# Performance work log

Hardware: AMD Instinct MI355X
Metric: run time of the kernel (lower is better)

Reference implementation:

```python
import jax, jax.numpy as jnp
import numpy as np

Q = 128


def _maxpool2(x):
    # 2x2 max pool, stride 2, NCHW
    return jax.lax.reduce_window(x, -jnp.inf, jax.lax.max,
                                 (1, 1, 2, 2), (1, 1, 2, 2), 'VALID')


def _conv(x, w, b):
    y = jax.lax.conv_general_dilated(x, w, window_strides=(1, 1), padding='VALID',
                                     dimension_numbers=('NCHW', 'OIHW', 'NCHW'))
    return y + b[None, :, None, None]


def setup_inputs() -> dict:
    key = jax.random.key(0)
    ks = jax.random.split(key, 16)
    B = 4096
    x = jax.random.normal(ks[0], (B, 1, 28, 28), dtype=jnp.float32)
    hash_idx1 = jax.random.randint(ks[1], (25,), 0, Q, dtype=jnp.int32)
    hash_idx2 = jax.random.randint(ks[2], (800,), 0, Q, dtype=jnp.int32)
    hash_idx3 = jax.random.randint(ks[3], (1024,), 0, Q, dtype=jnp.int32)
    # random +/-1 signs
    sgn1 = jnp.sign(jax.random.normal(ks[4], (25,), dtype=jnp.float32))
    sgn2 = jnp.sign(jax.random.normal(ks[5], (800,), dtype=jnp.float32))
    sgn3 = jnp.sign(jax.random.normal(ks[6], (1024,), dtype=jnp.float32))
    # compressed (sketched) parameters: one length-Q vector per output unit
    w1 = jax.random.normal(ks[7], (32, Q), dtype=jnp.float32) * 0.2
    b1 = jax.random.normal(ks[8], (32,), dtype=jnp.float32) * 0.05
    w2 = jax.random.normal(ks[9], (64, Q), dtype=jnp.float32) * 0.05
    b2 = jax.random.normal(ks[10], (64,), dtype=jnp.float32) * 0.05
    w3 = jax.random.normal(ks[11], (512, Q), dtype=jnp.float32) * 0.03
    b3 = jax.random.normal(ks[12], (512,), dtype=jnp.float32) * 0.05
    fc2_w = jax.random.normal(ks[13], (10, 512), dtype=jnp.float32) * 0.04
    fc2_b = jax.random.normal(ks[14], (10,), dtype=jnp.float32) * 0.05
    return {'x': x,
            'hash_idx1': hash_idx1, 'hash_idx2': hash_idx2, 'hash_idx3': hash_idx3,
            'sgn1': sgn1, 'sgn2': sgn2, 'sgn3': sgn3,
            'w1': w1, 'b1': b1, 'w2': w2, 'b2': b2, 'w3': w3, 'b3': b3,
            'fc2_w': fc2_w, 'fc2_b': fc2_b}


def reference(x, hash_idx1, hash_idx2, hash_idx3, sgn1, sgn2, sgn3,
              w1, b1, w2, b2, w3, b3, fc2_w, fc2_b):
    # SketchConv1: reconstruct dense weight via gather + sign flip
    wc1 = (w1[:, hash_idx1] * sgn1[None, :]).reshape(32, 1, 5, 5)
    h = jax.nn.relu(_maxpool2(_conv(x, wc1, b1)))          # (B,32,12,12)
    # SketchConv2
    wc2 = (w2[:, hash_idx2] * sgn2[None, :]).reshape(64, 32, 5, 5)
    h = jax.nn.relu(_maxpool2(_conv(h, wc2, b2)))          # (B,64,4,4)
    h = h.reshape(h.shape[0], -1)                          # (B,1024)
    # SketchLinear
    W3 = w3[:, hash_idx3] * sgn3[None, :]                  # (512,1024)
    h = jax.nn.relu(h @ W3.T + b3)                         # (B,512)
    logits = h @ fc2_w.T + fc2_b                           # (B,10)
    return jax.nn.log_softmax(logits, axis=1)
```

## Files before the change

kernel.cpp:

```cpp
#include <hip/hip_runtime.h>
#include <hip/hip_bf16.h>
#include <math.h>


typedef __attribute__((ext_vector_type(8))) short bf16x8;
typedef __attribute__((ext_vector_type(4))) float f32x4;

static __device__ inline ushort f2bfu(float v) {
    union { __hip_bfloat16 h; ushort u; } cv;
    cv.h = __float2bfloat16(v);
    return cv.u;
}


__global__ __launch_bounds__(256)
void k_reconstruct(const float* __restrict__ w1, const float* __restrict__ w2,
                   const float* __restrict__ w3,
                   const int* __restrict__ hi1, const int* __restrict__ hi2,
                   const int* __restrict__ hi3,
                   const float* __restrict__ s1, const float* __restrict__ s2,
                   const float* __restrict__ s3,
                   __hip_bfloat16* __restrict__ wc1f,
                   __hip_bfloat16* __restrict__ wc1s,
                   __hip_bfloat16* __restrict__ wc2f,
                   __hip_bfloat16* __restrict__ W3f) {
    const int t = blockIdx.x * blockDim.x + threadIdx.x;
    const int f = t >> 2;
    const int j0 = (t & 3) * 2;
    if (f < 256) {
        const bool shifted = f >= 128;
        const int u = f & 127;
        const int nt = u >> 6, lane = u & 63;
        const int quad = lane >> 4, l15 = lane & 15;
        const int oc = nt * 16 + l15;
        ushort rr[2];
        #pragma unroll
        for (int jj = 0; jj < 2; ++jj) {
            int tt = quad * 8 + j0 + jj;
            int ki = (tt * 43) >> 8;
            int kj = tt - 6 * ki;
            float v = 0.f;
            if (!shifted && ki < 5 && kj < 5) {
                int fi = ki * 5 + kj;
                v = w1[oc * 128 + hi1[fi]] * s1[fi];
            } else if (shifted && ki < 5 && kj >= 1 && kj <= 5) {
                int fi = ki * 5 + (kj - 1);
                v = w1[oc * 128 + hi1[fi]] * s1[fi];
            }
            rr[jj] = f2bfu(v);
        }
        *(uint*)((ushort*)(shifted ? wc1s : wc1f) + (size_t)u * 8 + j0) =
            (uint)rr[0] | ((uint)rr[1] << 16);
    } else if (f < 6656) {
        const int u = f - 256;
        const int l15 = u & 15, quad = (u >> 4) & 3;
        const int ntA = (u >> 6) & 3, tap = u >> 8;
        const int oc = ntA * 16 + l15;
        ushort rr[2];
        #pragma unroll
        for (int jj = 0; jj < 2; ++jj) {
            int ic = quad * 8 + j0 + jj;
            int fi = ic * 25 + tap;
            rr[jj] = f2bfu(w2[oc * 128 + hi2[fi]] * s2[fi]);
        }
        *(uint*)((ushort*)wc2f + (size_t)u * 8 + j0) =
            (uint)rr[0] | ((uint)rr[1] << 16);
    } else if (f < 72192) {
        const int u = f - 6656;
        const int l15 = u & 15, quad = (u >> 4) & 3;
        const int kt = (u >> 6) & 31, ntile = u >> 11;
        const int n = ntile * 16 + l15;
        ushort rr[2];
        #pragma unroll
        for (int jj = 0; jj < 2; ++jj) {
            int k = kt * 32 + quad * 8 + j0 + jj;
            rr[jj] = f2bfu(w3[n * 128 + hi3[k]] * s3[k]);
        }
        *(uint*)((ushort*)W3f + (size_t)u * 8 + j0) =
            (uint)rr[0] | ((uint)rr[1] << 16);
    }
}

__global__ __launch_bounds__(512, 6)
void k_conv(const float* __restrict__ x,
            const __hip_bfloat16* __restrict__ wc1f,
            const __hip_bfloat16* __restrict__ wc1s,
            const __hip_bfloat16* __restrict__ wc2f,
            const float* __restrict__ b1, const float* __restrict__ b2,
            __hip_bfloat16* __restrict__ h2) {
    __shared__ __align__(16) ushort s_xb[4 * 816];
    __shared__ __align__(16) ushort s_h1[16 * 1160];

    const int tid = threadIdx.x;
    const int b0 = blockIdx.x * 4;
    const int wave = tid >> 6, lane = tid & 63;
    const int l15 = lane & 15, quad = lane >> 4;

    {
        const float4* xg = (const float4*)(x + (size_t)b0 * 784);
        for (int i = tid; i < 784; i += 512) {
            float4 v = xg[i];
            int img = i / 196;
            int pos = (i - img * 196) * 4;
            ushort* dst = &s_xb[img * 816 + pos];
            dst[0] = f2bfu(v.x); dst[1] = f2bfu(v.y);
            dst[2] = f2bfu(v.z); dst[3] = f2bfu(v.w);
        }
        if (tid < 128) {
            int img = tid >> 5, k = tid & 31;
            s_xb[img * 816 + 784 + k] = 0;
        }
    }

    bf16x8 bw1[2], bw1s[2];
    float bb1[2];
    #pragma unroll
    for (int nt = 0; nt < 2; ++nt) {
        bw1[nt]  = *(const bf16x8*)((const ushort*)wc1f + (nt * 64 + lane) * 8);
        bw1s[nt] = *(const bf16x8*)((const ushort*)wc1s + (nt * 64 + lane) * 8);
        bb1[nt] = b1[nt * 16 + l15];
    }
    __syncthreads();

    {
        const int img = wave >> 1, half = wave & 1;
        const int sub = l15 & 3;
        const ushort* srcImg = s_xb + img * 816;
        int offr[4];
        #pragma unroll
        for (int r = 0; r < 4; ++r) {
            int t = quad * 8 + 2 * r;
            int row = (t * 43) >> 8;
            int col = t - 6 * row;
            offr[r] = row * 28 + col;
        }
        const int g0 = l15 >> 3, r0 = l15 & 7;
        #pragma unroll
        for (int ii = 0; ii < 18; ++ii) {
            const int i = half * 18 + ii;
            const int pb = 4 * i + (l15 >> 2);
            const int pi = (pb * 171) >> 11;
            const int pj = pb - 12 * pi;
            const int base_e = (2 * pi + (sub >> 1)) * 28 + 2 * pj;
            const ushort* p0 = srcImg + base_e;
            union { bf16x8 v; uint u[4]; } A;
            A.u[0] = *(const uint*)(p0 + offr[0]);
            A.u[1] = *(const uint*)(p0 + offr[1]);
            A.u[2] = *(const uint*)(p0 + offr[2]);
            A.u[3] = *(const uint*)(p0 + offr[3]);
            f32x4 z = {0.f, 0.f, 0.f, 0.f};
            f32x4 ce0 = __builtin_amdgcn_mfma_f32_16x16x32_bf16(A.v, bw1[0],  z, 0, 0, 0);
            f32x4 co0 = __builtin_amdgcn_mfma_f32_16x16x32_bf16(A.v, bw1s[0], z, 0, 0, 0);
            f32x4 ce1 = __builtin_amdgcn_mfma_f32_16x16x32_bf16(A.v, bw1[1],  z, 0, 0, 0);
            f32x4 co1 = __builtin_amdgcn_mfma_f32_16x16x32_bf16(A.v, bw1s[1], z, 0, 0, 0);
            const int pbo = 4 * i + quad;
            float m0 = fmaxf(fmaxf(ce0[0], co0[1]), fmaxf(ce0[2], co0[3]));
            float m1 = fmaxf(fmaxf(ce1[0], co1[1]), fmaxf(ce1[2], co1[3]));
            s_h1[(img * 4 + g0) * 1160 + pbo * 8 + r0]     = f2bfu(fmaxf(m0 + bb1[0], 0.f));
            s_h1[(img * 4 + 2 + g0) * 1160 + pbo * 8 + r0] = f2bfu(fmaxf(m1 + bb1[1], 0.f));
        }
    }
    __syncthreads();

    const int pr = wave >> 1, nh = wave & 1;
    const int sub2 = l15 & 3;
    const int ci2 = 2 * pr + (sub2 >> 1);
    const int cj2 = 2 * (l15 >> 2) + (sub2 & 1);
    const int posBase = (ci2 * 12 + cj2) * 8;

    f32x4 acc[4][2];
    float bb2[2];
    #pragma unroll
    for (int ntl = 0; ntl < 2; ++ntl) {
        bb2[ntl] = b2[(nh * 2 + ntl) * 16 + l15];
        #pragma unroll
        for (int img = 0; img < 4; ++img)
            acc[img][ntl] = (f32x4){0.f, 0.f, 0.f, 0.f};
    }

    #pragma unroll
    for (int tap = 0; tap < 25; ++tap) {
        const int ki = tap / 5, kj = tap % 5;
        const int off = (ki * 12 + kj) * 8;
        bf16x8 a[4];
        #pragma unroll
        for (int img = 0; img < 4; ++img)
            a[img] = *(const bf16x8*)&s_h1[(img * 4 + quad) * 1160 + posBase + off];
        #pragma unroll
        for (int ntl = 0; ntl < 2; ++ntl) {
            bf16x8 bf = *(const bf16x8*)((const ushort*)wc2f +
                          ((tap * 4 + nh * 2 + ntl) * 64 + lane) * 8);
            #pragma unroll
            for (int img = 0; img < 4; ++img)
                acc[img][ntl] = __builtin_amdgcn_mfma_f32_16x16x32_bf16(
                    a[img], bf, acc[img][ntl], 0, 0, 0);
        }
    }

    #pragma unroll
    for (int img = 0; img < 4; ++img)
        #pragma unroll
        for (int ntl = 0; ntl < 2; ++ntl) {
            f32x4 c = acc[img][ntl];
            float m = fmaxf(fmaxf(c[0], c[1]), fmaxf(c[2], c[3]));
            float v = fmaxf(m + bb2[ntl], 0.f);
            h2[(size_t)(b0 + img) * 1024 + ((nh * 2 + ntl) * 16 + l15) * 16 + pr * 4 + quad] =
                __float2bfloat16(v);
        }
}

__global__ __launch_bounds__(1024)
void k_fc(const __hip_bfloat16* __restrict__ A, const __hip_bfloat16* __restrict__ W3f,
          const float* __restrict__ b3, const float* __restrict__ fc2w,
          const float* __restrict__ fc2b, float* __restrict__ out) {
    __shared__ __align__(16) ushort s_A[16 * 1032];
    __shared__ float s_h3[16 * 516];

    const int tid = threadIdx.x;
    const int wave = tid >> 6, lane = tid & 63;
    const int l15 = lane & 15, quad = lane >> 4;
    const int mBase = blockIdx.x * 16;

    {
        const uint4* g = (const uint4*)(A + (size_t)(mBase + wave) * 1024);
        uint4 v0 = g[lane * 2], v1 = g[lane * 2 + 1];
        uint4* d = (uint4*)&s_A[wave * 1032 + lane * 16];
        d[0] = v0; d[1] = v1;
    }
    __syncthreads();

    f32x4 acc[2];
    acc[0] = (f32x4){0.f, 0.f, 0.f, 0.f};
    acc[1] = (f32x4){0.f, 0.f, 0.f, 0.f};

    const ushort* aP = &s_A[l15 * 1032 + quad * 8];
    const ushort* bP0 = (const ushort*)W3f + (((size_t)(wave * 2)     * 32) * 64 + lane) * 8;
    const ushort* bP1 = (const ushort*)W3f + (((size_t)(wave * 2 + 1) * 32) * 64 + lane) * 8;
    #pragma unroll 8
    for (int kt = 0; kt < 32; ++kt) {
        bf16x8 a = *(const bf16x8*)(aP + kt * 32);
        bf16x8 bf0 = *(const bf16x8*)(bP0 + kt * 512);
        bf16x8 bf1 = *(const bf16x8*)(bP1 + kt * 512);
        acc[0] = __builtin_amdgcn_mfma_f32_16x16x32_bf16(a, bf0, acc[0], 0, 0, 0);
        acc[1] = __builtin_amdgcn_mfma_f32_16x16x32_bf16(a, bf1, acc[1], 0, 0, 0);
    }

    #pragma unroll
    for (int ntl = 0; ntl < 2; ++ntl) {
        int col = wave * 32 + ntl * 16 + l15;
        float bb = b3[col];
        #pragma unroll
        for (int r = 0; r < 4; ++r)
            s_h3[(quad * 4 + r) * 516 + col] = fmaxf(acc[ntl][r] + bb, 0.f);
    }
    __syncthreads();

    const float* hrow = &s_h3[wave * 516];
    float4 h0 = *(const float4*)&hrow[lane * 8];
    float4 h1 = *(const float4*)&hrow[lane * 8 + 4];
    float lg[10];
    #pragma unroll
    for (int c = 0; c < 10; ++c) {
        float4 w0 = *(const float4*)&fc2w[c * 512 + lane * 8];
        float4 w1 = *(const float4*)&fc2w[c * 512 + lane * 8 + 4];
        float s = h0.x * w0.x + h0.y * w0.y + h0.z * w0.z + h0.w * w0.w
                + h1.x * w1.x + h1.y * w1.y + h1.z * w1.z + h1.w * w1.w;
        s += __shfl_down(s, 32);
        s += __shfl_down(s, 16);
        s += __shfl_down(s, 8);
        s += __shfl_down(s, 4);
        s += __shfl_down(s, 2);
        s += __shfl_down(s, 1);
        lg[c] = s;
    }
    if (lane == 0) {
        float mx = -1e30f;
        #pragma unroll
        for (int c = 0; c < 10; ++c) { lg[c] += fc2b[c]; mx = fmaxf(mx, lg[c]); }
        float sum = 0.f;
        #pragma unroll
        for (int c = 0; c < 10; ++c) sum += expf(lg[c] - mx);
        float lse = mx + logf(sum);
        #pragma unroll
        for (int c = 0; c < 10; ++c)
            out[(size_t)(mBase + wave) * 10 + c] = lg[c] - lse;
    }
}

extern "C" void kernel_launch(void* const* d_in, const int* in_sizes, int n_in,
                              void* d_out, int out_size, void* d_ws, size_t ws_size,
                              hipStream_t stream) {
    const float* x    = (const float*)d_in[0];
    const int*   hi1  = (const int*)d_in[1];
    const int*   hi2  = (const int*)d_in[2];
    const int*   hi3  = (const int*)d_in[3];
    const float* s1   = (const float*)d_in[4];
    const float* s2   = (const float*)d_in[5];
    const float* s3   = (const float*)d_in[6];
    const float* w1   = (const float*)d_in[7];
    const float* b1   = (const float*)d_in[8];
    const float* w2   = (const float*)d_in[9];
    const float* b2   = (const float*)d_in[10];
    const float* w3   = (const float*)d_in[11];
    const float* b3   = (const float*)d_in[12];
    const float* fc2w = (const float*)d_in[13];
    const float* fc2b = (const float*)d_in[14];
    float* out = (float*)d_out;

    const int B = in_sizes[0] / 784;

    char* ws = (char*)d_ws;
    __hip_bfloat16* wc1f = (__hip_bfloat16*)(ws + 0);
    __hip_bfloat16* wc1s = (__hip_bfloat16*)(ws + 2048);
    __hip_bfloat16* wc2f = (__hip_bfloat16*)(ws + 4096);
    __hip_bfloat16* W3f  = (__hip_bfloat16*)(ws + 106496);
    __hip_bfloat16* h2   = (__hip_bfloat16*)(ws + 1155072);

    k_reconstruct<<<1128, 256, 0, stream>>>(
        w1, w2, w3, hi1, hi2, hi3, s1, s2, s3, wc1f, wc1s, wc2f, W3f);
    k_conv<<<B / 4, 512, 0, stream>>>(x, wc1f, wc1s, wc2f, b1, b2, h2);
    k_fc<<<B / 16, 1024, 0, stream>>>(h2, W3f, b3, fc2w, fc2b, out);
}
```

Before: 146.0 us.

## Fold sketched FC1 hashing into conv epilogue, shrinking FC1 K from 1024 to 128

Because W3 = w3[:, hash] * sign, h @ W3.T equals (h scattered-and-signed into Q=128 buckets) @ w3.T. The conv kernel now accumulates its pooled outputs into 128 sketch buckets per image with shared-memory atomics and writes a 128-wide bf16 vector. FC1 then runs with K=128 against w3 converted directly to bf16, cutting the FC GEMM work, the h2 traffic and the weight reconstruction size by about 8x. The cost is extra syncs and LDS atomics in the conv epilogue, plus a different bf16 rounding point that slightly changes accuracy. The s_h1 row stride also changes.

```diff
diff --git a/kernel.cpp b/kernel.cpp
--- a/kernel.cpp
+++ b/kernel.cpp
@@ -17,13 +17,11 @@
 void k_reconstruct(const float* __restrict__ w1, const float* __restrict__ w2,
                    const float* __restrict__ w3,
                    const int* __restrict__ hi1, const int* __restrict__ hi2,
-                   const int* __restrict__ hi3,
                    const float* __restrict__ s1, const float* __restrict__ s2,
-                   const float* __restrict__ s3,
                    __hip_bfloat16* __restrict__ wc1f,
                    __hip_bfloat16* __restrict__ wc1s,
                    __hip_bfloat16* __restrict__ wc2f,
-                   __hip_bfloat16* __restrict__ W3f) {
+                   __hip_bfloat16* __restrict__ W3d) {
     const int t = blockIdx.x * blockDim.x + threadIdx.x;
     const int f = t >> 2;
     const int j0 = (t & 3) * 2;
@@ -65,18 +63,18 @@
         }
         *(uint*)((ushort*)wc2f + (size_t)u * 8 + j0) =
             (uint)rr[0] | ((uint)rr[1] << 16);
-    } else if (f < 72192) {
+    } else if (f < 14848) {
         const int u = f - 6656;
         const int l15 = u & 15, quad = (u >> 4) & 3;
-        const int kt = (u >> 6) & 31, ntile = u >> 11;
+        const int kt = (u >> 6) & 3, ntile = u >> 8;
         const int n = ntile * 16 + l15;
         ushort rr[2];
         #pragma unroll
         for (int jj = 0; jj < 2; ++jj) {
             int k = kt * 32 + quad * 8 + j0 + jj;
-            rr[jj] = f2bfu(w3[n * 128 + hi3[k]] * s3[k]);
-        }
-        *(uint*)((ushort*)W3f + (size_t)u * 8 + j0) =
+            rr[jj] = f2bfu(w3[n * 128 + k]);
+        }
+        *(uint*)((ushort*)W3d + (size_t)u * 8 + j0) =
             (uint)rr[0] | ((uint)rr[1] << 16);
     }
 }
@@ -87,9 +85,11 @@
             const __hip_bfloat16* __restrict__ wc1s,
             const __hip_bfloat16* __restrict__ wc2f,
             const float* __restrict__ b1, const float* __restrict__ b2,
+            const int* __restrict__ hi3, const float* __restrict__ s3,
             __hip_bfloat16* __restrict__ h2) {
     __shared__ __align__(16) ushort s_xb[4 * 816];
-    __shared__ __align__(16) ushort s_h1[16 * 1160];
+    __shared__ __align__(16) ushort s_h1[16 * 1184];
+    __shared__ float s_hb[4][128];
 
     const int tid = threadIdx.x;
     const int b0 = blockIdx.x * 4;
@@ -156,11 +156,13 @@
             const int pbo = 4 * i + quad;
             float m0 = fmaxf(fmaxf(ce0[0], co0[1]), fmaxf(ce0[2], co0[3]));
             float m1 = fmaxf(fmaxf(ce1[0], co1[1]), fmaxf(ce1[2], co1[3]));
-            s_h1[(img * 4 + g0) * 1160 + pbo * 8 + r0]     = f2bfu(fmaxf(m0 + bb1[0], 0.f));
-            s_h1[(img * 4 + 2 + g0) * 1160 + pbo * 8 + r0] = f2bfu(fmaxf(m1 + bb1[1], 0.f));
-        }
-    }
-    __syncthreads();
+            s_h1[(img * 4 + g0) * 1184 + pbo * 8 + r0]     = f2bfu(fmaxf(m0 + bb1[0], 0.f));
+            s_h1[(img * 4 + 2 + g0) * 1184 + pbo * 8 + r0] = f2bfu(fmaxf(m1 + bb1[1], 0.f));
+        }
+    }
+    __syncthreads();
+
+    if (tid < 512) ((float*)s_hb)[tid] = 0.f;
 
     const int pr = wave >> 1, nh = wave & 1;
     const int sub2 = l15 & 3;
@@ -185,7 +187,7 @@
         bf16x8 a[4];
         #pragma unroll
         for (int img = 0; img < 4; ++img)
-            a[img] = *(const bf16x8*)&s_h1[(img * 4 + quad) * 1160 + posBase + off];
+            a[img] = *(const bf16x8*)&s_h1[(img * 4 + quad) * 1184 + posBase + off];
         #pragma unroll
         for (int ntl = 0; ntl < 2; ++ntl) {
             bf16x8 bf = *(const bf16x8*)((const ushort*)wc2f +
@@ -197,23 +199,36 @@
         }
     }
 
-    #pragma unroll
-    for (int img = 0; img < 4; ++img)
-        #pragma unroll
-        for (int ntl = 0; ntl < 2; ++ntl) {
-            f32x4 c = acc[img][ntl];
-            float m = fmaxf(fmaxf(c[0], c[1]), fmaxf(c[2], c[3]));
-            float v = fmaxf(m + bb2[ntl], 0.f);
-            h2[(size_t)(b0 + img) * 1024 + ((nh * 2 + ntl) * 16 + l15) * 16 + pr * 4 + quad] =
-                __float2bfloat16(v);
-        }
+    __syncthreads();
+
+    const int k0 = ((nh * 2 + 0) * 16 + l15) * 16 + pr * 4 + quad;
+    const int k1 = ((nh * 2 + 1) * 16 + l15) * 16 + pr * 4 + quad;
+    const int q0 = hi3[k0], q1 = hi3[k1];
+    const float sg0 = s3[k0], sg1 = s3[k1];
+    #pragma unroll
+    for (int img = 0; img < 4; ++img) {
+        f32x4 c0 = acc[img][0];
+        float m0 = fmaxf(fmaxf(c0[0], c0[1]), fmaxf(c0[2], c0[3]));
+        float v0 = fmaxf(m0 + bb2[0], 0.f);
+        atomicAdd(&s_hb[img][q0], v0 * sg0);
+        f32x4 c1 = acc[img][1];
+        float m1 = fmaxf(fmaxf(c1[0], c1[1]), fmaxf(c1[2], c1[3]));
+        float v1 = fmaxf(m1 + bb2[1], 0.f);
+        atomicAdd(&s_hb[img][q1], v1 * sg1);
+    }
+    __syncthreads();
+
+    if (tid < 512) {
+        int img = tid >> 7, q = tid & 127;
+        h2[(size_t)(b0 + img) * 128 + q] = __float2bfloat16(s_hb[img][q]);
+    }
 }
 
 __global__ __launch_bounds__(1024)
-void k_fc(const __hip_bfloat16* __restrict__ A, const __hip_bfloat16* __restrict__ W3f,
+void k_fc(const __hip_bfloat16* __restrict__ A, const __hip_bfloat16* __restrict__ W3d,
           const float* __restrict__ b3, const float* __restrict__ fc2w,
           const float* __restrict__ fc2b, float* __restrict__ out) {
-    __shared__ __align__(16) ushort s_A[16 * 1032];
+    __shared__ __align__(16) ushort s_A[16 * 136];
     __shared__ float s_h3[16 * 516];
 
     const int tid = threadIdx.x;
@@ -222,10 +237,8 @@
     const int mBase = blockIdx.x * 16;
 
     {
-        const uint4* g = (const uint4*)(A + (size_t)(mBase + wave) * 1024);
-        uint4 v0 = g[lane * 2], v1 = g[lane * 2 + 1];
-        uint4* d = (uint4*)&s_A[wave * 1032 + lane * 16];
-        d[0] = v0; d[1] = v1;
+        const uint* g = (const uint*)(A + (size_t)(mBase + wave) * 128);
+        *(uint*)&s_A[wave * 136 + lane * 2] = g[lane];
     }
     __syncthreads();
 
@@ -233,11 +246,11 @@
     acc[0] = (f32x4){0.f, 0.f, 0.f, 0.f};
     acc[1] = (f32x4){0.f, 0.f, 0.f, 0.f};
 
-    const ushort* aP = &s_A[l15 * 1032 + quad * 8];
-    const ushort* bP0 = (const ushort*)W3f + (((size_t)(wave * 2)     * 32) * 64 + lane) * 8;
-    const ushort* bP1 = (const ushort*)W3f + (((size_t)(wave * 2 + 1) * 32) * 64 + lane) * 8;
-    #pragma unroll 8
-    for (int kt = 0; kt < 32; ++kt) {
+    const ushort* aP = &s_A[l15 * 136 + quad * 8];
+    const ushort* bP0 = (const ushort*)W3d + ((size_t)(wave * 2)     * 4 * 64 + lane) * 8;
+    const ushort* bP1 = (const ushort*)W3d + ((size_t)(wave * 2 + 1) * 4 * 64 + lane) * 8;
+    #pragma unroll
+    for (int kt = 0; kt < 4; ++kt) {
         bf16x8 a = *(const bf16x8*)(aP + kt * 32);
         bf16x8 bf0 = *(const bf16x8*)(bP0 + kt * 512);
         bf16x8 bf1 = *(const bf16x8*)(bP1 + kt * 512);
@@ -313,11 +326,11 @@
     __hip_bfloat16* wc1f = (__hip_bfloat16*)(ws + 0);
     __hip_bfloat16* wc1s = (__hip_bfloat16*)(ws + 2048);
     __hip_bfloat16* wc2f = (__hip_bfloat16*)(ws + 4096);
-    __hip_bfloat16* W3f  = (__hip_bfloat16*)(ws + 106496);
+    __hip_bfloat16* W3d  = (__hip_bfloat16*)(ws + 106496);
     __hip_bfloat16* h2   = (__hip_bfloat16*)(ws + 1155072);
 
-    k_reconstruct<<<1128, 256, 0, stream>>>(
-        w1, w2, w3, hi1, hi2, hi3, s1, s2, s3, wc1f, wc1s, wc2f, W3f);
-    k_conv<<<B / 4, 512, 0, stream>>>(x, wc1f, wc1s, wc2f, b1, b2, h2);
-    k_fc<<<B / 16, 1024, 0, stream>>>(h2, W3f, b3, fc2w, fc2b, out);
-}
+    k_reconstruct<<<232, 256, 0, stream>>>(
+        w1, w2, w3, hi1, hi2, s1, s2, wc1f, wc1s, wc2f, W3d);
+    k_conv<<<B / 4, 512, 0, stream>>>(x, wc1f, wc1s, wc2f, b1, b2, hi3, s3, h2);
+    k_fc<<<B / 16, 1024, 0, stream>>>(h2, W3d, b3, fc2w, fc2b, out);
+}
```

Measured after the change: 145.4 us. About the same (-0.4%).

## Sketch activations into hash buckets so the FC layer uses compact weights

Applied to the files above, without the earlier changes.

Instead of expanding the hashed linear weight to 512x1024, a per-bucket table of (index, sign) entries is built once. Each FC block folds its 1024 activations into 128 signed bucket sums, then multiplies them by the compact 512x128 w3. This cuts the FC matmul K dimension by 8x and shrinks the weight reconstruction work. The cost is a divergent, variable-length LDS gather loop per lane and an extra bf16 rounding of the bucket sums. The table caps each bucket at 32 entries, which silently drops entries if a bucket overflows.

```diff
diff --git a/kernel.cpp b/kernel.cpp
--- a/kernel.cpp
+++ b/kernel.cpp
@@ -10,6 +10,12 @@
     union { __hip_bfloat16 h; ushort u; } cv;
     cv.h = __float2bfloat16(v);
     return cv.u;
+}
+
+static __device__ inline float bfu2f(ushort u) {
+    union { ushort u; __hip_bfloat16 h; } cv;
+    cv.u = u;
+    return __bfloat162float(cv.h);
 }
 
 
@@ -23,7 +29,22 @@
                    __hip_bfloat16* __restrict__ wc1f,
                    __hip_bfloat16* __restrict__ wc1s,
                    __hip_bfloat16* __restrict__ wc2f,
-                   __hip_bfloat16* __restrict__ W3f) {
+                   __hip_bfloat16* __restrict__ W3d,
+                   int* __restrict__ cnt, uint* __restrict__ tab) {
+    if (blockIdx.x == 232) {
+        const int u = threadIdx.x;
+        if (u < 128) cnt[u] = 0;
+        __syncthreads();
+        #pragma unroll
+        for (int j = 0; j < 4; ++j) {
+            int k = u * 4 + j;
+            int q = hi3[k];
+            int p = atomicAdd(&cnt[q], 1);
+            if (p < 32)
+                tab[q * 32 + p] = (uint)k | ((uint)f2bfu(s3[k]) << 16);
+        }
+        return;
+    }
     const int t = blockIdx.x * blockDim.x + threadIdx.x;
     const int f = t >> 2;
     const int j0 = (t & 3) * 2;
@@ -65,18 +86,18 @@
         }
         *(uint*)((ushort*)wc2f + (size_t)u * 8 + j0) =
             (uint)rr[0] | ((uint)rr[1] << 16);
-    } else if (f < 72192) {
+    } else if (f < 14848) {
         const int u = f - 6656;
         const int l15 = u & 15, quad = (u >> 4) & 3;
-        const int kt = (u >> 6) & 31, ntile = u >> 11;
+        const int kt = (u >> 6) & 3, ntile = u >> 8;
         const int n = ntile * 16 + l15;
         ushort rr[2];
         #pragma unroll
         for (int jj = 0; jj < 2; ++jj) {
             int k = kt * 32 + quad * 8 + j0 + jj;
-            rr[jj] = f2bfu(w3[n * 128 + hi3[k]] * s3[k]);
-        }
-        *(uint*)((ushort*)W3f + (size_t)u * 8 + j0) =
+            rr[jj] = f2bfu(w3[n * 128 + k]);
+        }
+        *(uint*)((ushort*)W3d + (size_t)u * 8 + j0) =
             (uint)rr[0] | ((uint)rr[1] << 16);
     }
 }
@@ -210,10 +231,12 @@
 }
 
 __global__ __launch_bounds__(1024)
-void k_fc(const __hip_bfloat16* __restrict__ A, const __hip_bfloat16* __restrict__ W3f,
+void k_fc(const __hip_bfloat16* __restrict__ A, const __hip_bfloat16* __restrict__ W3d,
+          const int* __restrict__ cnt, const uint* __restrict__ tab,
           const float* __restrict__ b3, const float* __restrict__ fc2w,
           const float* __restrict__ fc2b, float* __restrict__ out) {
     __shared__ __align__(16) ushort s_A[16 * 1032];
+    __shared__ __align__(16) ushort s_Ab[16 * 136];
     __shared__ float s_h3[16 * 516];
 
     const int tid = threadIdx.x;
@@ -229,15 +252,33 @@
     }
     __syncthreads();
 
+    {
+        const ushort* arow = &s_A[wave * 1032];
+        uint pack[2];
+        #pragma unroll
+        for (int hh = 0; hh < 2; ++hh) {
+            int q = lane * 2 + hh;
+            int n = cnt[q];
+            float v = 0.f;
+            for (int i = 0; i < n; ++i) {
+                uint e = tab[q * 32 + i];
+                v += bfu2f(arow[e & 0xffff]) * bfu2f((ushort)(e >> 16));
+            }
+            pack[hh] = f2bfu(v);
+        }
+        *(uint*)&s_Ab[wave * 136 + lane * 2] = pack[0] | (pack[1] << 16);
+    }
+    __syncthreads();
+
     f32x4 acc[2];
     acc[0] = (f32x4){0.f, 0.f, 0.f, 0.f};
     acc[1] = (f32x4){0.f, 0.f, 0.f, 0.f};
 
-    const ushort* aP = &s_A[l15 * 1032 + quad * 8];
-    const ushort* bP0 = (const ushort*)W3f + (((size_t)(wave * 2)     * 32) * 64 + lane) * 8;
-    const ushort* bP1 = (const ushort*)W3f + (((size_t)(wave * 2 + 1) * 32) * 64 + lane) * 8;
-    #pragma unroll 8
-    for (int kt = 0; kt < 32; ++kt) {
+    const ushort* aP = &s_Ab[l15 * 136 + quad * 8];
+    const ushort* bP0 = (const ushort*)W3d + ((size_t)(wave * 2)     * 4 * 64 + lane) * 8;
+    const ushort* bP1 = (const ushort*)W3d + ((size_t)(wave * 2 + 1) * 4 * 64 + lane) * 8;
+    #pragma unroll
+    for (int kt = 0; kt < 4; ++kt) {
         bf16x8 a = *(const bf16x8*)(aP + kt * 32);
         bf16x8 bf0 = *(const bf16x8*)(bP0 + kt * 512);
         bf16x8 bf1 = *(const bf16x8*)(bP1 + kt * 512);
@@ -313,11 +354,13 @@
     __hip_bfloat16* wc1f = (__hip_bfloat16*)(ws + 0);
     __hip_bfloat16* wc1s = (__hip_bfloat16*)(ws + 2048);
     __hip_bfloat16* wc2f = (__hip_bfloat16*)(ws + 4096);
-    __hip_bfloat16* W3f  = (__hip_bfloat16*)(ws + 106496);
+    __hip_bfloat16* W3d  = (__hip_bfloat16*)(ws + 106496);
+    int*            cnt  = (int*)(ws + 237568);
+    uint*           tab  = (uint*)(ws + 238080);
     __hip_bfloat16* h2   = (__hip_bfloat16*)(ws + 1155072);
 
-    k_reconstruct<<<1128, 256, 0, stream>>>(
-        w1, w2, w3, hi1, hi2, hi3, s1, s2, s3, wc1f, wc1s, wc2f, W3f);
+    k_reconstruct<<<233, 256, 0, stream>>>(
+        w1, w2, w3, hi1, hi2, hi3, s1, s2, s3, wc1f, wc1s, wc2f, W3d, cnt, tab);
     k_conv<<<B / 4, 512, 0, stream>>>(x, wc1f, wc1s, wc2f, b1, b2, h2);
-    k_fc<<<B / 16, 1024, 0, stream>>>(h2, W3f, b3, fc2w, fc2b, out);
-}
+    k_fc<<<B / 16, 1024, 0, stream>>>(h2, W3d, cnt, tab, b3, fc2w, fc2b, out);
+}
```

Result: faster. 141.3 us (-3.2%).
